# Performance work log

Hardware: AMD Instinct MI355X
Metric: run time of the kernel (lower is better)

Reference implementation:

```python
import jax, jax.numpy as jnp
import numpy as np

N = 50000       # nodes
E = 500000      # edges (before self-loops)
F_IN = 128      # node feature dim
F_E = 16        # edge feature dim
H = 8           # heads (conv1, conv2)
C1 = 32         # 256 // 8
C2 = 16         # 128 // 8
OUT = 1         # conv3 output channels (1 head, concat=False)
NS = 0.2        # leaky_relu negative slope
EPS = 1e-5      # batchnorm eps


def setup_inputs() -> dict:
    key = jax.random.key(0)
    ks = jax.random.split(key, 32)
    r = lambda k, s: jax.random.normal(k, s, jnp.float32) * 0.1
    inp = {
        'x': jax.random.normal(ks[0], (N, F_IN), jnp.float32),
        'edge_index': jax.random.randint(ks[1], (2, E), 0, N, jnp.int32),
        'edge_attr': jax.random.normal(ks[2], (E, F_E), jnp.float32),
        # conv1 (share_weights=True -> single lin)
        'W1': r(ks[3], (F_IN, H * C1)), 'b1': jnp.zeros((H * C1,), jnp.float32),
        'We1': r(ks[4], (F_E, H * C1)), 'att1': r(ks[5], (H, C1)),
        'bo1': jnp.zeros((H * C1,), jnp.float32),
        'g1': jnp.ones((H * C1,), jnp.float32), 'bt1': jnp.zeros((H * C1,), jnp.float32),
        # conv2 (share_weights=True)
        'W2': r(ks[6], (H * C1, H * C2)), 'b2': jnp.zeros((H * C2,), jnp.float32),
        'We2': r(ks[7], (F_E, H * C2)), 'att2': r(ks[8], (H, C2)),
        'bo2': jnp.zeros((H * C2,), jnp.float32),
        'g2': jnp.ones((H * C2,), jnp.float32), 'bt2': jnp.zeros((H * C2,), jnp.float32),
        # conv3 (share_weights=False -> separate lin_l / lin_r; 1 head, concat=False)
        'W3l': r(ks[9], (H * C2, OUT)), 'b3l': jnp.zeros((OUT,), jnp.float32),
        'W3r': r(ks[10], (H * C2, OUT)), 'b3r': jnp.zeros((OUT,), jnp.float32),
        'We3': r(ks[11], (F_E, OUT)), 'att3': r(ks[12], (1, OUT)),
        'bo3': jnp.zeros((OUT,), jnp.float32),
    }
    return inp


def _gatv2(x, src, dst, eattr, Wl, bl, Wr, br, We, att, bo, heads, ch, concat):
    """One GATv2Conv layer (PyG semantics), edges already include self-loops."""
    n = x.shape[0]
    xl = (x @ Wl + bl).reshape(n, heads, ch)              # source transform
    xr = (x @ Wr + br).reshape(n, heads, ch)              # target transform
    e = (eattr @ We).reshape(-1, heads, ch)               # edge transform (no bias)
    m = xl[src] + xr[dst] + e                             # [Etot, H, C]
    logit = jnp.einsum('ehc,hc->eh', jax.nn.leaky_relu(m, NS), att)
    lmax = jax.ops.segment_max(logit, dst, num_segments=n)
    ex = jnp.exp(logit - lmax[dst])
    denom = jax.ops.segment_sum(ex, dst, num_segments=n)
    alpha = ex / (denom[dst] + 1e-16)                     # segment softmax over dst
    out = jax.ops.segment_sum(alpha[:, :, None] * xl[src], dst, num_segments=n)
    out = out.reshape(n, heads * ch) if concat else out.mean(axis=1)
    return out + bo


def _bn(x, g, b):
    mu = x.mean(axis=0)
    var = ((x - mu) ** 2).mean(axis=0)
    return g * (x - mu) * jax.lax.rsqrt(var + EPS) + b


def reference(x, edge_index, edge_attr, W1, b1, We1, att1, bo1, g1, bt1,
              W2, b2, We2, att2, bo2, g2, bt2,
              W3l, b3l, W3r, b3r, We3, att3, bo3):
    n = x.shape[0]
    # add_self_loops=True with fill_value='mean' for edge_attr (PyG default)
    loop = jnp.arange(n, dtype=edge_index.dtype)
    src = jnp.concatenate([edge_index[0], loop])
    dst = jnp.concatenate([edge_index[1], loop])
    ea = jnp.concatenate([edge_attr,
                          jnp.broadcast_to(edge_attr.mean(axis=0), (n, edge_attr.shape[1]))], axis=0)

    h = _gatv2(x, src, dst, ea, W1, b1, W1, b1, We1, att1, bo1, H, C1, True)
    h = jax.nn.elu(_bn(h, g1, bt1))
    h = _gatv2(h, src, dst, ea, W2, b2, W2, b2, We2, att2, bo2, H, C2, True)
    h = jax.nn.elu(_bn(h, g2, bt2))
    out = _gatv2(h, src, dst, ea, W3l, b3l, W3r, b3r, We3, att3, bo3, 1, OUT, False)
    return out  # [N, 1]
```

## Files before the change

kernel.cpp:

```cpp
#include <hip/hip_runtime.h>

typedef unsigned short u16;
typedef __attribute__((ext_vector_type(4))) float f32x4;
typedef __attribute__((ext_vector_type(2))) float f32x2;
typedef __attribute__((ext_vector_type(8))) short bf16x8;

constexpr int Nn  = 50000;
constexpr int Ee  = 500000;
constexpr int ET  = Nn + Ee;
constexpr int FIN = 128;
constexpr int FE  = 16;
constexpr int Hh  = 8;
constexpr int C1  = 32, HC1 = 256;
constexpr int C2  = 16, HC2 = 128;
constexpr float NS  = 0.2f;
constexpr float EPS = 1e-5f;

__device__ __forceinline__ float b2f(u16 u) { return __uint_as_float(((unsigned)u) << 16); }
__device__ __forceinline__ u16 f2b(float f) {
  unsigned u = __float_as_uint(f);
  u += 0x7FFF + ((u >> 16) & 1);
  return (u16)(u >> 16);
}
__device__ __forceinline__ f32x2 ldbf2(const u16* p) {
  ushort2 u = *reinterpret_cast<const ushort2*>(p);
  return (f32x2){b2f(u.x), b2f(u.y)};
}
__device__ __forceinline__ void stbf2(u16* p, f32x2 v) {
  ushort2 u; u.x = f2b(v.x); u.y = f2b(v.y);
  *reinterpret_cast<ushort2*>(p) = u;
}

__global__ void k_ea_mean(const float* __restrict__ ea, float* __restrict__ ea_mean) {
  __shared__ float s[256];
  int f  = threadIdx.x & 15;
  int r0 = (threadIdx.x >> 4) + blockIdx.x * 16;
  float acc = 0.f;
  for (int e = r0; e < Ee; e += gridDim.x * 16) acc += ea[e * FE + f];
  s[threadIdx.x] = acc;
  __syncthreads();
  if (threadIdx.x < 16) {
    float t = 0.f;
    for (int r = 0; r < 16; r++) t += s[r * 16 + threadIdx.x];
    atomicAdd(&ea_mean[threadIdx.x], t * (1.f / Ee));
  }
}

__global__ void k_deg(const int* __restrict__ ei, int* __restrict__ deg) {
  int e = blockIdx.x * 256 + threadIdx.x;
  if (e >= ET) return;
  int d = (e < Ee) ? ei[Ee + e] : (e - Ee);
  if ((unsigned)d >= (unsigned)Nn) d = 0;
  atomicAdd(&deg[d], 1);
}

__global__ __launch_bounds__(1024) void k_scan(const int* __restrict__ deg, int* __restrict__ rowptr) {
  const int T = 1024;
  int t = threadIdx.x;
  const int CH = (Nn + T - 1) / T;
  int base = t * CH;
  int sum = 0;
  for (int i = 0; i < CH; i++) {
    int idx = base + i;
    if (idx < Nn) sum += deg[idx];
  }
  __shared__ int s[T];
  s[t] = sum;
  __syncthreads();
  for (int off = 1; off < T; off <<= 1) {
    int v = (t >= off) ? s[t - off] : 0;
    __syncthreads();
    s[t] += v;
    __syncthreads();
  }
  int run = (t == 0) ? 0 : s[t - 1];
  for (int i = 0; i < CH; i++) {
    int idx = base + i;
    if (idx < Nn) { rowptr[idx] = run; run += deg[idx]; }
  }
  if (t == T - 1) rowptr[Nn] = run;
}

__global__ void k_scatter(const int* __restrict__ ei, const int* __restrict__ rowptr,
                          int* __restrict__ cursor, int2* __restrict__ epack) {
  int e = blockIdx.x * 256 + threadIdx.x;
  if (e >= ET) return;
  int s, d;
  if (e < Ee) { s = ei[e]; d = ei[Ee + e]; } else { s = d = e - Ee; }
  if ((unsigned)s >= (unsigned)Nn) s = 0;
  if ((unsigned)d >= (unsigned)Nn) d = 0;
  int pos = rowptr[d] + atomicAdd(&cursor[d], 1);
  epack[pos] = make_int2(s, e);
}

__global__ void k_bn_coef(const float* __restrict__ sum, const float* __restrict__ sq,
                          const float* __restrict__ g, const float* __restrict__ bt,
                          float2* __restrict__ coef, int HC) {
  int ch = threadIdx.x;
  if (ch >= HC) return;
  float mu = sum[ch] * (1.f / Nn);
  float var = sq[ch] * (1.f / Nn) - mu * mu;
  float rs = rsqrtf(var + EPS);
  float sc = g[ch] * rs;
  coef[ch] = make_float2(sc, bt[ch] - sc * mu);
}

template <int KK, int NN, typename AT, bool FUSE>
__global__ __launch_bounds__(256) void k_gemm_mfma(const AT* __restrict__ A, const float* __restrict__ W,
                                                   const float* __restrict__ bias, u16* __restrict__ C,
                                                   const float2* __restrict__ coef, int M) {
  constexpr int WT = KK + 8;
  __shared__ u16 Wt[64 * WT];
  int tid = threadIdx.x;
  int col0 = blockIdx.x * 64;
  int row0 = blockIdx.y * 64;
  for (int idx = tid; idx < KK * 64; idx += 256) {
    int k = idx >> 6, c = idx & 63;
    Wt[c * WT + k] = f2b(W[(size_t)k * NN + col0 + c]);
  }
  __syncthreads();
  int lane = tid & 63;
  int w = tid >> 6;
  int mr = lane & 15, quad = lane >> 4;
  int row = row0 + w * 16 + mr;
  f32x4 acc[4];
#pragma unroll
  for (int t = 0; t < 4; t++) acc[t] = (f32x4){0.f, 0.f, 0.f, 0.f};
  union Frag { bf16x8 v; u16 u[8]; };
  for (int kb = 0; kb < KK; kb += 32) {
    Frag a;
    if (row < M) {
      if constexpr (sizeof(AT) == 4) {
        const float* ap = (const float*)&A[(size_t)row * KK + kb + quad * 8];
        float4 a0 = *reinterpret_cast<const float4*>(ap);
        float4 a1 = *reinterpret_cast<const float4*>(ap + 4);
        a.u[0] = f2b(a0.x); a.u[1] = f2b(a0.y); a.u[2] = f2b(a0.z); a.u[3] = f2b(a0.w);
        a.u[4] = f2b(a1.x); a.u[5] = f2b(a1.y); a.u[6] = f2b(a1.z); a.u[7] = f2b(a1.w);
      } else {
        a.v = *reinterpret_cast<const bf16x8*>(&A[(size_t)row * KK + kb + quad * 8]);
        if constexpr (FUSE) {
          int k0 = kb + quad * 8;
#pragma unroll
          for (int j = 0; j < 8; j++) {
            float2 c2 = coef[k0 + j];
            float y = b2f(a.u[j]) * c2.x + c2.y;
            y = y > 0.f ? y : __expf(y) - 1.f;
            a.u[j] = f2b(y);
          }
        }
      }
    } else {
#pragma unroll
      for (int j = 0; j < 8; j++) a.u[j] = 0;
    }
#pragma unroll
    for (int t = 0; t < 4; t++) {
      const bf16x8* bp = reinterpret_cast<const bf16x8*>(&Wt[(t * 16 + mr) * WT + kb + quad * 8]);
      acc[t] = __builtin_amdgcn_mfma_f32_16x16x32_bf16(a.v, *bp, acc[t], 0, 0, 0);
    }
  }
  int orow = row0 + w * 16 + quad * 4;
#pragma unroll
  for (int t = 0; t < 4; t++) {
    int col = col0 + t * 16 + mr;
    float bs = bias[col];
#pragma unroll
    for (int r = 0; r < 4; r++) {
      int rr = orow + r;
      if (rr < M) C[(size_t)rr * NN + col] = f2b(acc[t][r] + bs);
    }
  }
}

template <int HC, int C, int WPN>
__global__ __launch_bounds__(256) void k_node_attn(
    const int* __restrict__ rowptr, const int2* __restrict__ epack,
    const u16* __restrict__ xl, const float* __restrict__ We, const float* __restrict__ att,
    const float* __restrict__ edge_attr, const float* __restrict__ ea_mean,
    const float* __restrict__ bo, u16* __restrict__ out) {
  int lane = threadIdx.x & 63;
  int gwid = (blockIdx.x << 2) + (threadIdx.x >> 6);
  int nwaves = gridDim.x << 2;
  int w = gwid % WPN;
  int i0 = gwid / WPN;
  int istride = nwaves / WPN;
  int c0 = w * 128 + lane * 2;
  f32x2 w2[FE];
#pragma unroll
  for (int k = 0; k < FE; k++) {
    float2 t = *reinterpret_cast<const float2*>(&We[k * HC + c0]);
    w2[k] = (f32x2){t.x, t.y};
  }
  float at0 = att[c0], at1 = att[c0 + 1];
  f32x2 ews2 = {0.f, 0.f};
#pragma unroll
  for (int k = 0; k < FE; k++) ews2 += ea_mean[k] * w2[k];
  float b0 = bo[c0], b1 = bo[c0 + 1];
  constexpr int RED = C / 2;
  constexpr int UN = 4;

  auto edge_ew = [&](int eid) -> f32x2 {
    if (eid < Ee) {
      const float4* ep = reinterpret_cast<const float4*>(&edge_attr[(size_t)eid * FE]);
      f32x2 a = {0.f, 0.f};
#pragma unroll
      for (int k4 = 0; k4 < 4; k4++) {
        float4 u = ep[k4];
        a += u.x * w2[4 * k4 + 0];
        a += u.y * w2[4 * k4 + 1];
        a += u.z * w2[4 * k4 + 2];
        a += u.w * w2[4 * k4 + 3];
      }
      return a;
    }
    return ews2;
  };

  for (int i = i0; i < Nn; i += istride) {
    int p0 = rowptr[i], p1 = rowptr[i + 1];
    f32x2 xd = ldbf2(&xl[(size_t)i * HC + c0]);
    float m = -1e30f, l = 0.f;
    f32x2 acc = {0.f, 0.f};
    int p = p0;
    for (; p + UN <= p1; p += UN) {
      int sA[UN], eA[UN];
#pragma unroll
      for (int j = 0; j < UN; j++) {
        int2 se = epack[p + j];
        sA[j] = __builtin_amdgcn_readfirstlane(se.x);
        eA[j] = __builtin_amdgcn_readfirstlane(se.y);
      }
      f32x2 xs[UN];
#pragma unroll
      for (int j = 0; j < UN; j++)
        xs[j] = ldbf2(&xl[(size_t)sA[j] * HC + c0]);
      f32x2 ew[UN];
#pragma unroll
      for (int j = 0; j < UN; j++) ew[j] = edge_ew(eA[j]);
      float part[UN];
#pragma unroll
      for (int j = 0; j < UN; j++) {
        f32x2 t = xs[j] + xd + ew[j];
        float t0 = t.x > 0.f ? t.x : NS * t.x;
        float t1 = t.y > 0.f ? t.y : NS * t.y;
        float pt = t0 * at0 + t1 * at1;
#pragma unroll
        for (int off = 1; off < RED; off <<= 1) pt += __shfl_xor(pt, off);
        part[j] = pt;
      }
      float mn = m;
#pragma unroll
      for (int j = 0; j < UN; j++) mn = fmaxf(mn, part[j]);
      float sc = __expf(m - mn);
      float a[UN], asum = 0.f;
      f32x2 ax = {0.f, 0.f};
#pragma unroll
      for (int j = 0; j < UN; j++) {
        a[j] = __expf(part[j] - mn);
        asum += a[j];
        ax += a[j] * xs[j];
      }
      l = l * sc + asum;
      acc = acc * sc + ax;
      m = mn;
    }
    for (; p < p1; p++) {
      int2 se = epack[p];
      int s = __builtin_amdgcn_readfirstlane(se.x);
      int eid = __builtin_amdgcn_readfirstlane(se.y);
      f32x2 ew = edge_ew(eid);
      f32x2 xs = ldbf2(&xl[(size_t)s * HC + c0]);
      f32x2 t = xs + xd + ew;
      float t0 = t.x > 0.f ? t.x : NS * t.x;
      float t1 = t.y > 0.f ? t.y : NS * t.y;
      float pt = t0 * at0 + t1 * at1;
#pragma unroll
      for (int off = 1; off < RED; off <<= 1) pt += __shfl_xor(pt, off);
      float mn = fmaxf(m, pt);
      float sc = __expf(m - mn);
      float a = __expf(pt - mn);
      l = l * sc + a;
      acc = acc * sc + a * xs;
      m = mn;
    }
    float inv = 1.f / (l + 1e-16f);
    f32x2 v = {acc.x * inv + b0, acc.y * inv + b1};
    stbf2(&out[(size_t)i * HC + c0], v);
  }
}

template <int HC>
__global__ void k_bn_stats(const u16* __restrict__ x, float* __restrict__ sum, float* __restrict__ sq) {
  long e0 = (long)blockIdx.x * 256 + threadIdx.x;
  long stride = (long)gridDim.x * 256;
  float s = 0.f, s2 = 0.f;
  for (long e = e0; e < (long)Nn * HC; e += stride) {
    float v = b2f(x[e]);
    s += v; s2 += v * v;
  }
  int ch = (int)(e0 % HC);
  atomicAdd(&sum[ch], s);
  atomicAdd(&sq[ch], s2);
}

__global__ __launch_bounds__(256) void k_gemv3(const u16* __restrict__ h2,
                                               const float2* __restrict__ coef,
                                               const float* __restrict__ W3l, const float* __restrict__ b3l,
                                               const float* __restrict__ W3r, const float* __restrict__ b3r,
                                               float* __restrict__ xl3, float* __restrict__ xr3) {
  int lane = threadIdx.x & 63;
  int i = (blockIdx.x << 2) + (threadIdx.x >> 6);
  if (i >= Nn) return;
  float2 ca = coef[lane], cb = coef[64 + lane];
  float a = b2f(h2[(long)i * HC2 + lane]) * ca.x + ca.y;
  a = a > 0.f ? a : __expf(a) - 1.f;
  float b = b2f(h2[(long)i * HC2 + 64 + lane]) * cb.x + cb.y;
  b = b > 0.f ? b : __expf(b) - 1.f;
  float pl = a * W3l[lane] + b * W3l[64 + lane];
  float pr = a * W3r[lane] + b * W3r[64 + lane];
  for (int o = 1; o < 64; o <<= 1) { pl += __shfl_xor(pl, o); pr += __shfl_xor(pr, o); }
  if (lane == 0) { xl3[i] = pl + b3l[0]; xr3[i] = pr + b3r[0]; }
}

__global__ __launch_bounds__(256) void k_final3(
    const int* __restrict__ rowptr, const int2* __restrict__ epack,
    const float* __restrict__ xl3, const float* __restrict__ xr3,
    const float* __restrict__ We3, const float* __restrict__ att3,
    const float* __restrict__ edge_attr, const float* __restrict__ ea_mean,
    const float* __restrict__ bo3, float* __restrict__ out) {
  int lane = threadIdx.x & 63;
  int i = (blockIdx.x << 2) + (threadIdx.x >> 6);
  if (i >= Nn) return;
  float we[FE];
#pragma unroll
  for (int k4 = 0; k4 < 4; k4++) {
    float4 u = reinterpret_cast<const float4*>(We3)[k4];
    we[4 * k4] = u.x; we[4 * k4 + 1] = u.y; we[4 * k4 + 2] = u.z; we[4 * k4 + 3] = u.w;
  }
  float at = att3[0];
  float ews = 0.f;
#pragma unroll
  for (int k = 0; k < FE; k++) ews += ea_mean[k] * we[k];
  float xd = xr3[i];
  int p0 = rowptr[i], p1 = rowptr[i + 1];
  float m = -1e30f, l = 0.f, o = 0.f;
  for (int p = p0 + lane; p < p1; p += 64) {
    int2 se = epack[p];
    int s = se.x, eid = se.y;
    float ew;
    if (eid < Ee) {
      const float4* ep = reinterpret_cast<const float4*>(&edge_attr[(size_t)eid * FE]);
      ew = 0.f;
#pragma unroll
      for (int k4 = 0; k4 < 4; k4++) {
        float4 u = ep[k4];
        ew += u.x * we[4 * k4] + u.y * we[4 * k4 + 1] + u.z * we[4 * k4 + 2] + u.w * we[4 * k4 + 3];
      }
    } else ew = ews;
    float xsv = xl3[s];
    float t = xsv + xd + ew;
    float v = t > 0.f ? t : NS * t;
    float logit = v * at;
    float mn = fmaxf(m, logit);
    float sc = __expf(m - mn);
    float a = __expf(logit - mn);
    l = l * sc + a;
    o = o * sc + a * xsv;
    m = mn;
  }
  float M = m;
#pragma unroll
  for (int off = 1; off < 64; off <<= 1) M = fmaxf(M, __shfl_xor(M, off));
  float adj = __expf(m - M);
  float lw = l * adj, ow = o * adj;
#pragma unroll
  for (int off = 1; off < 64; off <<= 1) { lw += __shfl_xor(lw, off); ow += __shfl_xor(ow, off); }
  if (lane == 0) out[i] = ow / (lw + 1e-16f) + bo3[0];
}

extern "C" void kernel_launch(void* const* d_in, const int* in_sizes, int n_in,
                              void* d_out, int out_size, void* d_ws, size_t ws_size,
                              hipStream_t stream) {
  const float* x    = (const float*)d_in[0];
  const int*   ei   = (const int*)d_in[1];
  const float* ea   = (const float*)d_in[2];
  const float* W1   = (const float*)d_in[3];
  const float* b1   = (const float*)d_in[4];
  const float* We1  = (const float*)d_in[5];
  const float* att1 = (const float*)d_in[6];
  const float* bo1  = (const float*)d_in[7];
  const float* g1   = (const float*)d_in[8];
  const float* bt1  = (const float*)d_in[9];
  const float* W2   = (const float*)d_in[10];
  const float* b2   = (const float*)d_in[11];
  const float* We2  = (const float*)d_in[12];
  const float* att2 = (const float*)d_in[13];
  const float* bo2  = (const float*)d_in[14];
  const float* g2   = (const float*)d_in[15];
  const float* bt2  = (const float*)d_in[16];
  const float* W3l  = (const float*)d_in[17];
  const float* b3l  = (const float*)d_in[18];
  const float* W3r  = (const float*)d_in[19];
  const float* b3r  = (const float*)d_in[20];
  const float* We3  = (const float*)d_in[21];
  const float* att3 = (const float*)d_in[22];
  const float* bo3  = (const float*)d_in[23];
  float* out = (float*)d_out;

  char* ws = (char*)d_ws;
  size_t off = 0;
  auto alloc = [&](size_t bytes) -> void* {
    void* p = ws + off;
    off = (off + bytes + 255) & ~(size_t)255;
    return p;
  };
  int*    deg     = (int*)alloc((size_t)Nn * 4);
  int*    rowptr  = (int*)alloc((size_t)(Nn + 1) * 4);
  int*    cursor  = (int*)alloc((size_t)Nn * 4);
  int2*   epack   = (int2*)alloc((size_t)ET * 8);
  float*  ea_mean = (float*)alloc((size_t)FE * 4);
  float*  bn_sum  = (float*)alloc(256 * 4);
  float*  bn_sq   = (float*)alloc(256 * 4);
  float2* bncoef  = (float2*)alloc(256 * 8);
  float*  xl3     = (float*)alloc((size_t)Nn * 4);
  float*  xr3     = (float*)alloc((size_t)Nn * 4);
  u16*    xlA     = (u16*)alloc((size_t)Nn * 256 * 2);
  u16*    hB      = (u16*)alloc((size_t)Nn * 256 * 2);

  hipMemsetAsync(deg, 0, (size_t)Nn * 4, stream);
  hipMemsetAsync(cursor, 0, (size_t)Nn * 4, stream);
  hipMemsetAsync(ea_mean, 0, (size_t)FE * 4, stream);

  k_ea_mean<<<400, 256, 0, stream>>>(ea, ea_mean);
  k_deg<<<(ET + 255) / 256, 256, 0, stream>>>(ei, deg);
  k_scan<<<1, 1024, 0, stream>>>(deg, rowptr);
  k_scatter<<<(ET + 255) / 256, 256, 0, stream>>>(ei, rowptr, cursor, epack);

  k_gemm_mfma<FIN, HC1, float, false><<<dim3(HC1 / 64, (Nn + 63) / 64), 256, 0, stream>>>(
      x, W1, b1, xlA, nullptr, Nn);
  k_node_attn<HC1, C1, 2><<<2048, 256, 0, stream>>>(rowptr, epack, xlA, We1, att1,
                                                    ea, ea_mean, bo1, hB);
  hipMemsetAsync(bn_sum, 0, 256 * 4, stream);
  hipMemsetAsync(bn_sq, 0, 256 * 4, stream);
  k_bn_stats<HC1><<<256, 256, 0, stream>>>(hB, bn_sum, bn_sq);
  k_bn_coef<<<1, 256, 0, stream>>>(bn_sum, bn_sq, g1, bt1, bncoef, HC1);

  k_gemm_mfma<HC1, HC2, u16, true><<<dim3(HC2 / 64, (Nn + 63) / 64), 256, 0, stream>>>(
      hB, W2, b2, xlA, bncoef, Nn);
  k_node_attn<HC2, C2, 1><<<2048, 256, 0, stream>>>(rowptr, epack, xlA, We2, att2,
                                                    ea, ea_mean, bo2, hB);
  hipMemsetAsync(bn_sum, 0, 256 * 4, stream);
  hipMemsetAsync(bn_sq, 0, 256 * 4, stream);
  k_bn_stats<HC2><<<256, 256, 0, stream>>>(hB, bn_sum, bn_sq);
  k_bn_coef<<<1, 256, 0, stream>>>(bn_sum, bn_sq, g2, bt2, bncoef, HC2);

  k_gemv3<<<(Nn + 3) / 4, 256, 0, stream>>>(hB, bncoef, W3l, b3l, W3r, b3r, xl3, xr3);
  k_final3<<<(Nn + 3) / 4, 256, 0, stream>>>(rowptr, epack, xl3, xr3, We3, att3,
                                             ea, ea_mean, bo3, out);
}
```

Before: 775.8 us.

## Unroll attention loop to 8 with masked tail, shrink final3 groups, deterministic BN partials

Result: slower. 987.7 us (+27.3%).

```diff
diff --git a/kernel.cpp b/kernel.cpp
--- a/kernel.cpp
+++ b/kernel.cpp
@@ -15,6 +15,7 @@
 constexpr int C2  = 16, HC2 = 128;
 constexpr float NS  = 0.2f;
 constexpr float EPS = 1e-5f;
+constexpr int BNB = 256;
 
 __device__ __forceinline__ float b2f(u16 u) { return __uint_as_float(((unsigned)u) << 16); }
 __device__ __forceinline__ u16 f2b(float f) {
@@ -93,13 +94,30 @@
   epack[pos] = make_int2(s, e);
 }
 
-__global__ void k_bn_coef(const float* __restrict__ sum, const float* __restrict__ sq,
+template <int HC>
+__global__ void k_bn_stats(const u16* __restrict__ x, float* __restrict__ psum, float* __restrict__ psq) {
+  int b = blockIdx.x, tid = threadIdx.x;
+  long e0 = (long)b * 256 + tid;
+  long stride = (long)BNB * 256;
+  float s = 0.f, s2 = 0.f;
+  for (long e = e0; e < (long)Nn * HC; e += stride) {
+    float v = b2f(x[e]);
+    s += v; s2 += v * v;
+  }
+  psum[b * 256 + tid] = s;
+  psq[b * 256 + tid] = s2;
+}
+
+__global__ void k_bn_coef(const float* __restrict__ psum, const float* __restrict__ psq,
                           const float* __restrict__ g, const float* __restrict__ bt,
                           float2* __restrict__ coef, int HC) {
   int ch = threadIdx.x;
   if (ch >= HC) return;
-  float mu = sum[ch] * (1.f / Nn);
-  float var = sq[ch] * (1.f / Nn) - mu * mu;
+  float s = 0.f, s2 = 0.f;
+  for (int b = 0; b < BNB; b++)
+    for (int r = ch; r < 256; r += HC) { s += psum[b * 256 + r]; s2 += psq[b * 256 + r]; }
+  float mu = s * (1.f / Nn);
+  float var = s2 * (1.f / Nn) - mu * mu;
   float rs = rsqrtf(var + EPS);
   float sc = g[ch] * rs;
   coef[ch] = make_float2(sc, bt[ch] - sc * mu);
@@ -197,7 +215,7 @@
   for (int k = 0; k < FE; k++) ews2 += ea_mean[k] * w2[k];
   float b0 = bo[c0], b1 = bo[c0 + 1];
   constexpr int RED = C / 2;
-  constexpr int UN = 4;
+  constexpr int UN = 8;
 
   auto edge_ew = [&](int eid) -> f32x2 {
     if (eid < Ee) {
@@ -221,12 +239,12 @@
     f32x2 xd = ldbf2(&xl[(size_t)i * HC + c0]);
     float m = -1e30f, l = 0.f;
     f32x2 acc = {0.f, 0.f};
-    int p = p0;
-    for (; p + UN <= p1; p += UN) {
+    for (int p = p0; p < p1; p += UN) {
       int sA[UN], eA[UN];
 #pragma unroll
       for (int j = 0; j < UN; j++) {
-        int2 se = epack[p + j];
+        int pj = (p + j < p1) ? p + j : p1 - 1;
+        int2 se = epack[pj];
         sA[j] = __builtin_amdgcn_readfirstlane(se.x);
         eA[j] = __builtin_amdgcn_readfirstlane(se.y);
       }
@@ -234,73 +252,38 @@
 #pragma unroll
       for (int j = 0; j < UN; j++)
         xs[j] = ldbf2(&xl[(size_t)sA[j] * HC + c0]);
-      f32x2 ew[UN];
-#pragma unroll
-      for (int j = 0; j < UN; j++) ew[j] = edge_ew(eA[j]);
       float part[UN];
 #pragma unroll
       for (int j = 0; j < UN; j++) {
-        f32x2 t = xs[j] + xd + ew[j];
+        f32x2 ew = edge_ew(eA[j]);
+        f32x2 t = xs[j] + xd + ew;
         float t0 = t.x > 0.f ? t.x : NS * t.x;
         float t1 = t.y > 0.f ? t.y : NS * t.y;
         float pt = t0 * at0 + t1 * at1;
 #pragma unroll
         for (int off = 1; off < RED; off <<= 1) pt += __shfl_xor(pt, off);
-        part[j] = pt;
+        part[j] = (p + j < p1) ? pt : -1e30f;
       }
       float mn = m;
 #pragma unroll
       for (int j = 0; j < UN; j++) mn = fmaxf(mn, part[j]);
       float sc = __expf(m - mn);
-      float a[UN], asum = 0.f;
+      float asum = 0.f;
       f32x2 ax = {0.f, 0.f};
 #pragma unroll
       for (int j = 0; j < UN; j++) {
-        a[j] = __expf(part[j] - mn);
-        asum += a[j];
-        ax += a[j] * xs[j];
+        float a = __expf(part[j] - mn);
+        asum += a;
+        ax += a * xs[j];
       }
       l = l * sc + asum;
       acc = acc * sc + ax;
-      m = mn;
-    }
-    for (; p < p1; p++) {
-      int2 se = epack[p];
-      int s = __builtin_amdgcn_readfirstlane(se.x);
-      int eid = __builtin_amdgcn_readfirstlane(se.y);
-      f32x2 ew = edge_ew(eid);
-      f32x2 xs = ldbf2(&xl[(size_t)s * HC + c0]);
-      f32x2 t = xs + xd + ew;
-      float t0 = t.x > 0.f ? t.x : NS * t.x;
-      float t1 = t.y > 0.f ? t.y : NS * t.y;
-      float pt = t0 * at0 + t1 * at1;
-#pragma unroll
-      for (int off = 1; off < RED; off <<= 1) pt += __shfl_xor(pt, off);
-      float mn = fmaxf(m, pt);
-      float sc = __expf(m - mn);
-      float a = __expf(pt - mn);
-      l = l * sc + a;
-      acc = acc * sc + a * xs;
       m = mn;
     }
     float inv = 1.f / (l + 1e-16f);
     f32x2 v = {acc.x * inv + b0, acc.y * inv + b1};
     stbf2(&out[(size_t)i * HC + c0], v);
   }
-}
-
-template <int HC>
-__global__ void k_bn_stats(const u16* __restrict__ x, float* __restrict__ sum, float* __restrict__ sq) {
-  long e0 = (long)blockIdx.x * 256 + threadIdx.x;
-  long stride = (long)gridDim.x * 256;
-  float s = 0.f, s2 = 0.f;
-  for (long e = e0; e < (long)Nn * HC; e += stride) {
-    float v = b2f(x[e]);
-    s += v; s2 += v * v;
-  }
-  int ch = (int)(e0 % HC);
-  atomicAdd(&sum[ch], s);
-  atomicAdd(&sq[ch], s2);
 }
 
 __global__ __launch_bounds__(256) void k_gemv3(const u16* __restrict__ h2,
@@ -328,8 +311,9 @@
     const float* __restrict__ We3, const float* __restrict__ att3,
     const float* __restrict__ edge_attr, const float* __restrict__ ea_mean,
     const float* __restrict__ bo3, float* __restrict__ out) {
-  int lane = threadIdx.x & 63;
-  int i = (blockIdx.x << 2) + (threadIdx.x >> 6);
+  int tid = threadIdx.x;
+  int sub = tid & 15;
+  int i = blockIdx.x * 16 + (tid >> 4);
   if (i >= Nn) return;
   float we[FE];
 #pragma unroll
@@ -344,7 +328,7 @@
   float xd = xr3[i];
   int p0 = rowptr[i], p1 = rowptr[i + 1];
   float m = -1e30f, l = 0.f, o = 0.f;
-  for (int p = p0 + lane; p < p1; p += 64) {
+  for (int p = p0 + sub; p < p1; p += 16) {
     int2 se = epack[p];
     int s = se.x, eid = se.y;
     float ew;
@@ -370,12 +354,12 @@
   }
   float M = m;
 #pragma unroll
-  for (int off = 1; off < 64; off <<= 1) M = fmaxf(M, __shfl_xor(M, off));
+  for (int off = 1; off < 16; off <<= 1) M = fmaxf(M, __shfl_xor(M, off));
   float adj = __expf(m - M);
   float lw = l * adj, ow = o * adj;
 #pragma unroll
-  for (int off = 1; off < 64; off <<= 1) { lw += __shfl_xor(lw, off); ow += __shfl_xor(ow, off); }
-  if (lane == 0) out[i] = ow / (lw + 1e-16f) + bo3[0];
+  for (int off = 1; off < 16; off <<= 1) { lw += __shfl_xor(lw, off); ow += __shfl_xor(ow, off); }
+  if (sub == 0) out[i] = ow / (lw + 1e-16f) + bo3[0];
 }
 
 extern "C" void kernel_launch(void* const* d_in, const int* in_sizes, int n_in,
@@ -419,8 +403,8 @@
   int*    cursor  = (int*)alloc((size_t)Nn * 4);
   int2*   epack   = (int2*)alloc((size_t)ET * 8);
   float*  ea_mean = (float*)alloc((size_t)FE * 4);
-  float*  bn_sum  = (float*)alloc(256 * 4);
-  float*  bn_sq   = (float*)alloc(256 * 4);
+  float*  psum    = (float*)alloc((size_t)BNB * 256 * 4);
+  float*  psq     = (float*)alloc((size_t)BNB * 256 * 4);
   float2* bncoef  = (float2*)alloc(256 * 8);
   float*  xl3     = (float*)alloc((size_t)Nn * 4);
   float*  xr3     = (float*)alloc((size_t)Nn * 4);
@@ -440,21 +424,17 @@
       x, W1, b1, xlA, nullptr, Nn);
   k_node_attn<HC1, C1, 2><<<2048, 256, 0, stream>>>(rowptr, epack, xlA, We1, att1,
                                                     ea, ea_mean, bo1, hB);
-  hipMemsetAsync(bn_sum, 0, 256 * 4, stream);
-  hipMemsetAsync(bn_sq, 0, 256 * 4, stream);
-  k_bn_stats<HC1><<<256, 256, 0, stream>>>(hB, bn_sum, bn_sq);
-  k_bn_coef<<<1, 256, 0, stream>>>(bn_sum, bn_sq, g1, bt1, bncoef, HC1);
+  k_bn_stats<HC1><<<BNB, 256, 0, stream>>>(hB, psum, psq);
+  k_bn_coef<<<1, 256, 0, stream>>>(psum, psq, g1, bt1, bncoef, HC1);
 
   k_gemm_mfma<HC1, HC2, u16, true><<<dim3(HC2 / 64, (Nn + 63) / 64), 256, 0, stream>>>(
       hB, W2, b2, xlA, bncoef, Nn);
   k_node_attn<HC2, C2, 1><<<2048, 256, 0, stream>>>(rowptr, epack, xlA, We2, att2,
                                                     ea, ea_mean, bo2, hB);
-  hipMemsetAsync(bn_sum, 0, 256 * 4, stream);
-  hipMemsetAsync(bn_sq, 0, 256 * 4, stream);
-  k_bn_stats<HC2><<<256, 256, 0, stream>>>(hB, bn_sum, bn_sq);
-  k_bn_coef<<<1, 256, 0, stream>>>(bn_sum, bn_sq, g2, bt2, bncoef, HC2);
+  k_bn_stats<HC2><<<BNB, 256, 0, stream>>>(hB, psum, psq);
+  k_bn_coef<<<1, 256, 0, stream>>>(psum, psq, g2, bt2, bncoef, HC2);
 
   k_gemv3<<<(Nn + 3) / 4, 256, 0, stream>>>(hB, bncoef, W3l, b3l, W3r, b3r, xl3, xr3);
-  k_final3<<<(Nn + 3) / 4, 256, 0, stream>>>(rowptr, epack, xl3, xr3, We3, att3,
-                                             ea, ea_mean, bo3, out);
-}
+  k_final3<<<(Nn + 15) / 16, 256, 0, stream>>>(rowptr, epack, xl3, xr3, We3, att3,
+                                               ea, ea_mean, bo3, out);
+}
```
